# Performance work log

Hardware: AMD Instinct MI355X
Metric: run time of the kernel (lower is better)

Reference implementation:

```python
import jax, jax.numpy as jnp
import numpy as np

TEMP = 0.07
BASE_TEMP = 0.07
LOSS_WEIGHT = 0.5
BN_EPS = 1e-5

N, C_IN, H, W = 8, 512, 128, 128
FEAT_DIM = 256
N_ANCHOR, N_VIEW = 152, 26  # total_classes, n_view from max_samples=4096


def _embed(x, W1, b1, gamma, beta, W2, b2):
    # x: [N, C, H, W]; 1x1 conv -> BatchNorm (batch stats, training mode) -> ReLU -> 1x1 conv -> L2 norm over channel
    h = jnp.einsum('nchw,dc->ndhw', x, W1) + b1[None, :, None, None]
    mu = h.mean(axis=(0, 2, 3), keepdims=True)
    var = h.var(axis=(0, 2, 3), keepdims=True)
    h = (h - mu) * jax.lax.rsqrt(var + BN_EPS)
    h = h * gamma[None, :, None, None] + beta[None, :, None, None]
    h = jax.nn.relu(h)
    z = jnp.einsum('nchw,dc->ndhw', h, W2) + b2[None, :, None, None]
    nrm = jnp.sqrt(jnp.sum(z * z, axis=1, keepdims=True))
    return z / jnp.maximum(nrm, 1e-12)


def _contrastive(fS, fT, labels):
    # fS, fT: [A, V, d]; labels: [A]
    A, V, d = fS.shape
    anchor = jnp.transpose(fS, (1, 0, 2)).reshape(V * A, d)  # cat(unbind(dim=1))
    contrast = jax.lax.stop_gradient(jnp.transpose(fT, (1, 0, 2)).reshape(V * A, d))
    logits = (anchor @ contrast.T) / TEMP  # [M, M]
    logits = logits - jax.lax.stop_gradient(logits.max(axis=1, keepdims=True))
    base = (labels[:, None] == labels[None, :]).astype(logits.dtype)  # [A, A]
    mask = jnp.tile(base, (V, V))  # repeat(anchor_count, contrast_count)
    neg_mask = 1.0 - mask
    M = V * A
    mask = mask * (1.0 - jnp.eye(M, dtype=logits.dtype))  # remove self-pairs
    exp_l = jnp.exp(logits)
    neg = (exp_l * neg_mask).sum(axis=1, keepdims=True)
    log_prob = logits - jnp.log(exp_l + neg)
    mean_log_prob_pos = (mask * log_prob).sum(axis=1) / (mask.sum(axis=1) + 1e-6)
    return (-(TEMP / BASE_TEMP) * mean_log_prob_pos).mean()


def setup_inputs() -> dict:
    key = jax.random.key(0)
    ks = jax.random.split(key, 16)
    inp = {
        'preds_S': jax.random.normal(ks[0], (N, C_IN, H, W), jnp.float32),
        'preds_T': jax.random.normal(ks[1], (N, C_IN, H, W), jnp.float32),
        'sample_batch': jax.random.randint(ks[2], (N_ANCHOR,), 0, N, jnp.int32),
        'sample_idx': jax.random.randint(ks[3], (N_ANCHOR, N_VIEW), 0, H * W, jnp.int32),
        'labels_': jax.random.randint(ks[4], (N_ANCHOR,), 0, 19, jnp.int32),
    }
    def conv_params(k, cin, cout):
        k1, k2 = jax.random.split(k)
        return (jax.random.normal(k1, (cout, cin), jnp.float32) * 0.02,
                jnp.zeros((cout,), jnp.float32))
    for pfx, kw, kb in (('s', ks[5], ks[6]), ('t', ks[7], ks[8])):
        W1, b1 = conv_params(kw, C_IN, C_IN)
        W2, b2 = conv_params(kb, C_IN, FEAT_DIM)
        inp[f'{pfx}_W1'], inp[f'{pfx}_b1'] = W1, b1
        inp[f'{pfx}_gamma'] = jnp.ones((C_IN,), jnp.float32)
        inp[f'{pfx}_beta'] = jnp.zeros((C_IN,), jnp.float32)
        inp[f'{pfx}_W2'], inp[f'{pfx}_b2'] = W2, b2
    return inp


def reference(preds_S, preds_T, sample_batch, sample_idx, labels_,
              s_W1, s_b1, s_gamma, s_beta, s_W2, s_b2,
              t_W1, t_b1, t_gamma, t_beta, t_W2, t_b2):
    zS = _embed(preds_S, s_W1, s_b1, s_gamma, s_beta, s_W2, s_b2)
    zT = _embed(preds_T, t_W1, t_b1, t_gamma, t_beta, t_W2, t_b2)
    n, d, h, w = zS.shape
    fS = jnp.transpose(zS, (0, 2, 3, 1)).reshape(n, h * w, d)
    fT = jnp.transpose(zT, (0, 2, 3, 1)).reshape(n, h * w, d)
    # hard-anchor gather: [A, V, d]
    fS_ = fS[sample_batch[:, None], sample_idx]
    fT_ = fT[sample_batch[:, None], sample_idx]
    loss = _contrastive(fS_, fT_, labels_) + _contrastive(fT_, fS_, labels_)
    return LOSS_WEIGHT * loss
```

## Files before the change

### kernel.cpp

```cpp
#include <hip/hip_runtime.h>
#include <hip/hip_bf16.h>

#define A_N 152
#define V_N 26
#define M_N 3952
#define M_PAD 3968
#define CIN 512
#define FDIM 256
#define HW_SZ 16384
#define P_TOT 131072.0f
#define TEMP_INV 14.285714285714286f
#define NGRP 2048
#define LCAP 64
#define PCAP 768

typedef __attribute__((ext_vector_type(8))) short bf16x8;
typedef __attribute__((ext_vector_type(4))) float f32x4;

static __device__ __forceinline__ short f2bf(float x){
  union { float f; unsigned u; } v; v.f = x;
  unsigned r = (v.u + 0x7FFFu + ((v.u >> 16) & 1u)) >> 16;
  return (short)r;
}

static __device__ __forceinline__ bf16x8 ldfrag(const short* __restrict__ base, int ld,
                                                int row, int k, int lane){
  return *(const bf16x8*)(base + (size_t)(row + (lane & 15)) * ld + k + ((lane >> 4) << 3));
}

static __device__ __forceinline__ bf16x8 ldfragP(const short* __restrict__ base,
                                                 int dtile, int ktile, int lane){
  return *(const bf16x8*)(base + ((((size_t)dtile << 4) + ktile) << 9) + (lane << 3));
}

static __device__ __forceinline__ void cvt4(short* __restrict__ lds, float4 v,
                                            int px, int tid){
  lds[(px+0)*512 + (tid ^ (((px+0)&7)<<3))] = f2bf(v.x);
  lds[(px+1)*512 + (tid ^ (((px+1)&7)<<3))] = f2bf(v.y);
  lds[(px+2)*512 + (tid ^ (((px+2)&7)<<3))] = f2bf(v.z);
  lds[(px+3)*512 + (tid ^ (((px+3)&7)<<3))] = f2bf(v.w);
}

__global__ void castw_kernel(const float* __restrict__ a0, short* __restrict__ o0,
                             const float* __restrict__ a1, short* __restrict__ o1,
                             const float* __restrict__ a2, short* __restrict__ o2,
                             const float* __restrict__ a3, short* __restrict__ o3){
  const float* a; short* o; int n;
  switch (blockIdx.y){
    case 0: a = a0; o = o0; n = CIN*CIN; break;
    case 1: a = a1; o = o1; n = CIN*CIN; break;
    case 2: a = a2; o = o2; n = FDIM*CIN; break;
    default: a = a3; o = o3; n = FDIM*CIN; break;
  }
  int i = blockIdx.x * 256 + threadIdx.x;
  if (i >= n) return;
  if (blockIdx.y < 2){
    int j  = i & 7;
    int ln = (i >> 3) & 63;
    int kt = (i >> 9) & 15;
    int dt = i >> 13;
    int row = dt * 16 + (ln & 15);
    int col = kt * 32 + ((ln >> 4) << 3) + j;
    o[i] = f2bf(a[row * CIN + col]);
  } else {
    o[i] = f2bf(a[i]);
  }
}

__global__ __launch_bounds__(64) void build_lists_kernel(
    const int* __restrict__ sb, const int* __restrict__ si,
    int* __restrict__ counts, int* __restrict__ lists){
  int m = blockIdx.x * 64 + threadIdx.x;
  if (m >= M_N) return;
  int a = m % A_N, v = m / A_N;
  int pix = si[a * V_N + v];
  int g = sb[a] * 256 + (pix >> 6);
  int slot = atomicAdd(&counts[g], 1);
  if (slot < LCAP) lists[g * LCAP + slot] = m | ((pix & 63) << 16);
}

__global__ __launch_bounds__(512, 2) void stats_kernel(
    const float* __restrict__ xS, const float* __restrict__ xT,
    const short* __restrict__ w1S, const short* __restrict__ w1T,
    float* __restrict__ stats,
    const int* __restrict__ counts, const int* __restrict__ lists,
    short* __restrict__ xsS, short* __restrict__ xsT){
  __shared__ short lds[128 * 512];
  const int t = blockIdx.y;
  const float* __restrict__ x = t ? xT : xS;
  const short* __restrict__ w1 = t ? w1T : w1S;
  float* sums = stats + t * 1024;
  short* __restrict__ xs = t ? xsT : xsS;

  const int tid  = threadIdx.x;
  const int lane = tid & 63;
  const int wave = tid >> 6;

  float rs[4] = {0.f,0.f,0.f,0.f};
  float rq[4] = {0.f,0.f,0.f,0.f};

  for (int it = 0; it < 4; ++it){
    const int T   = blockIdx.x + it * 256;
    const int n   = T >> 7;
    const int hw0 = (T & 127) << 7;
    const float* src = x + ((size_t)(n * CIN + tid)) * HW_SZ + hw0;

    const int g0 = T * 2, g1 = g0 + 1;
    int cnt0 = counts[g0]; if (cnt0 > LCAP) cnt0 = LCAP;
    int cnt1 = counts[g1]; if (cnt1 > LCAP) cnt1 = LCAP;

    #pragma unroll
    for (int ch = 0; ch < 8; ++ch){
      float4 v0 = *(const float4*)(src + ch * 16 +  0);
      float4 v1 = *(const float4*)(src + ch * 16 +  4);
      float4 v2 = *(const float4*)(src + ch * 16 +  8);
      float4 v3 = *(const float4*)(src + ch * 16 + 12);
      cvt4(lds, v0, ch * 16 +  0, tid);
      cvt4(lds, v1, ch * 16 +  4, tid);
      cvt4(lds, v2, ch * 16 +  8, tid);
      cvt4(lds, v3, ch * 16 + 12, tid);
    }
    __syncthreads();

    f32x4 acc[8][4] = {};
    {
      bf16x8 c0 = ldfragP(w1, wave*4 + 0, 0, lane);
      bf16x8 c1 = ldfragP(w1, wave*4 + 1, 0, lane);
      bf16x8 c2 = ldfragP(w1, wave*4 + 2, 0, lane);
      bf16x8 c3 = ldfragP(w1, wave*4 + 3, 0, lane);
      for (int kt = 0; kt < 16; ++kt){
        const int kn = (kt + 1) & 15;
        bf16x8 n0 = ldfragP(w1, wave*4 + 0, kn, lane);
        bf16x8 n1 = ldfragP(w1, wave*4 + 1, kn, lane);
        bf16x8 n2 = ldfragP(w1, wave*4 + 2, kn, lane);
        bf16x8 n3 = ldfragP(w1, wave*4 + 3, kn, lane);
        const int kk = kt << 5;
        #pragma unroll
        for (int pi = 0; pi < 8; ++pi){
          int px = pi*16 + (lane & 15);
          int c  = (kk + ((lane >> 4) << 3)) ^ ((px & 7) << 3);
          bf16x8 af = *(const bf16x8*)(lds + px*512 + c);
          acc[pi][0] = __builtin_amdgcn_mfma_f32_16x16x32_bf16(af, c0, acc[pi][0], 0, 0, 0);
          acc[pi][1] = __builtin_amdgcn_mfma_f32_16x16x32_bf16(af, c1, acc[pi][1], 0, 0, 0);
          acc[pi][2] = __builtin_amdgcn_mfma_f32_16x16x32_bf16(af, c2, acc[pi][2], 0, 0, 0);
          acc[pi][3] = __builtin_amdgcn_mfma_f32_16x16x32_bf16(af, c3, acc[pi][3], 0, 0, 0);
        }
        c0 = n0; c1 = n1; c2 = n2; c3 = n3;
      }
    }
    #pragma unroll
    for (int di = 0; di < 4; ++di){
      float s = 0.f, q2 = 0.f;
      #pragma unroll
      for (int pi = 0; pi < 8; ++pi)
        #pragma unroll
        for (int r = 0; r < 4; ++r){ float vv = acc[pi][di][r]; s += vv; q2 += vv*vv; }
      rs[di] += s; rq[di] += q2;
    }

    for (int s = 0; s < cnt0; ++s){
      int e = lists[g0 * LCAP + s];
      int m = e & 0xFFFF, px = e >> 16;
      xs[(size_t)m * CIN + tid] = lds[px * 512 + (tid ^ ((px & 7) << 3))];
    }
    for (int s = 0; s < cnt1; ++s){
      int e = lists[g1 * LCAP + s];
      int m = e & 0xFFFF, px = (e >> 16) + 64;
      xs[(size_t)m * CIN + tid] = lds[px * 512 + (tid ^ ((px & 7) << 3))];
    }
    __syncthreads();
  }
  #pragma unroll
  for (int di = 0; di < 4; ++di){
    float s = rs[di], q2 = rq[di];
    s  += __shfl_xor(s, 16, 64);  s  += __shfl_xor(s, 32, 64);
    q2 += __shfl_xor(q2, 16, 64); q2 += __shfl_xor(q2, 32, 64);
    if ((lane & 48) == 0){
      int d = wave * 64 + di*16 + lane;
      atomicAdd(&sums[d], s);
      atomicAdd(&sums[512 + d], q2);
    }
  }
}

__global__ __launch_bounds__(256) void conv1_kernel(
    const short* __restrict__ xsS, const short* __restrict__ xsT,
    const short* __restrict__ w1S, const short* __restrict__ w1T,
    const float* __restrict__ stats,
    const float* __restrict__ gS, const float* __restrict__ bS,
    const float* __restrict__ gT, const float* __restrict__ bT,
    short* __restrict__ hrS, short* __restrict__ hrT){
  const int t = blockIdx.z;
  const short* xs = t ? xsT : xsS;
  const short* w1 = t ? w1T : w1S;
  const float* sums  = stats + t * 1024;
  const float* gamma = t ? gT : gS;
  const float* beta  = t ? bT : bS;
  short* hr = t ? hrT : hrS;

  const int lane = threadIdx.x & 63;
  const int wave = threadIdx.x >> 6;
  const int m0 = blockIdx.x * 16;
  const int dt0 = (blockIdx.y * 4 + wave) * 4;
  const int d0  = dt0 * 16;

  f32x4 acc[4] = {};
  for (int kk = 0; kk < CIN; kk += 32){
    bf16x8 a = ldfrag(xs, CIN, m0, kk, lane);
    #pragma unroll
    for (int di = 0; di < 4; ++di){
      bf16x8 b = ldfragP(w1, dt0 + di, kk >> 5, lane);
      acc[di] = __builtin_amdgcn_mfma_f32_16x16x32_bf16(a, b, acc[di], 0, 0, 0);
    }
  }
  const float invP = 1.f / P_TOT;
  #pragma unroll
  for (int di = 0; di < 4; ++di){
    int d = d0 + di*16 + (lane & 15);
    float mu  = sums[d] * invP;
    float var = sums[512 + d] * invP - mu * mu;
    float sc  = gamma[d] * rsqrtf(var + 1e-5f);
    float sh  = beta[d] - mu * sc;
    #pragma unroll
    for (int r = 0; r < 4; ++r){
      int m = m0 + ((lane >> 4) << 2) + r;
      float v = fmaxf(acc[di][r] * sc + sh, 0.f);
      hr[(size_t)m * CIN + d] = f2bf(v);
    }
  }
}

__global__ __launch_bounds__(256) void conv2_kernel(
    const short* __restrict__ hrS, const short* __restrict__ hrT,
    const short* __restrict__ w2S, const short* __restrict__ w2T,
    const float* __restrict__ b2S, const float* __restrict__ b2T,
    short* __restrict__ fS, short* __restrict__ fT){
  __shared__ float ssum[4][16];
  const int t = blockIdx.y;
  const short* hr = t ? hrT : hrS;
  const short* w2 = t ? w2T : w2S;
  const float* b2 = t ? b2T : b2S;
  short* f = t ? fT : fS;

  const int lane = threadIdx.x & 63;
  const int wave = threadIdx.x >> 6;
  const int m0 = blockIdx.x * 16;
  const int e0 = wave * 64;

  f32x4 acc[4] = {};
  for (int kk = 0; kk < CIN; kk += 32){
    bf16x8 a = ldfrag(hr, CIN, m0, kk, lane);
    #pragma unroll
    for (int ei = 0; ei < 4; ++ei){
      bf16x8 b = ldfrag(w2, CIN, e0 + ei*16, kk, lane);
      acc[ei] = __builtin_amdgcn_mfma_f32_16x16x32_bf16(a, b, acc[ei], 0, 0, 0);
    }
  }
  float z[4][4];
  float part[4] = {0.f,0.f,0.f,0.f};
  #pragma unroll
  for (int ei = 0; ei < 4; ++ei){
    int e = e0 + ei*16 + (lane & 15);
    float bb = b2[e];
    #pragma unroll
    for (int r = 0; r < 4; ++r){
      float v = acc[ei][r] + bb;
      z[ei][r] = v;
      part[r] += v * v;
    }
  }
  #pragma unroll
  for (int r = 0; r < 4; ++r){
    float p = part[r];
    p += __shfl_xor(p, 1, 64); p += __shfl_xor(p, 2, 64);
    p += __shfl_xor(p, 4, 64); p += __shfl_xor(p, 8, 64);
    part[r] = p;
  }
  if ((lane & 15) == 0){
    #pragma unroll
    for (int r = 0; r < 4; ++r) ssum[wave][((lane >> 4) << 2) + r] = part[r];
  }
  __syncthreads();
  #pragma unroll
  for (int r = 0; r < 4; ++r){
    int mrow = ((lane >> 4) << 2) + r;
    float tot = ssum[0][mrow] + ssum[1][mrow] + ssum[2][mrow] + ssum[3][mrow];
    float sc = 1.f / fmaxf(sqrtf(tot), 1e-12f);
    #pragma unroll
    for (int ei = 0; ei < 4; ++ei){
      int e = e0 + ei*16 + (lane & 15);
      f[(size_t)(m0 + mrow) * FDIM + e] = f2bf(z[ei][r] * sc);
    }
  }
}

__global__ __launch_bounds__(256) void fused_kernel(
    const short* __restrict__ fS, const short* __restrict__ fT,
    const int* __restrict__ labels, float* __restrict__ out){
  __shared__ unsigned char lab[M_N];
  __shared__ float stash[16][PCAP];
  __shared__ int   scnt[16];
  __shared__ float redm[4][16], reds[4][16];
  __shared__ float fmx[16], fng[16];

  const short* fa = blockIdx.y ? fT : fS;
  const short* fb = blockIdx.y ? fS : fT;
  const int tid  = threadIdx.x;
  const int lane = tid & 63;
  const int wave = tid >> 6;
  const int m0 = blockIdx.x * 16;

  for (int j = tid; j < M_N; j += 256) lab[j] = (unsigned char)labels[j % A_N];
  if (tid < 16) scnt[tid] = 0;
  __syncthreads();

  const int rbase = (lane >> 4) << 2;
  int labrow[4];
  #pragma unroll
  for (int r = 0; r < 4; ++r) labrow[r] = lab[m0 + rbase + r];

  float pm[4]   = {-3.4e38f,-3.4e38f,-3.4e38f,-3.4e38f};
  float psum[4] = {0.f,0.f,0.f,0.f};

  for (int nt = wave; nt < 62; nt += 4){
    const int n0 = nt * 64;
    f32x4 acc[4] = {};
    for (int kk = 0; kk < FDIM; kk += 32){
      bf16x8 a = ldfrag(fa, FDIM, m0, kk, lane);
      #pragma unroll
      for (int ni = 0; ni < 4; ++ni){
        bf16x8 b = ldfrag(fb, FDIM, n0 + ni*16, kk, lane);
        acc[ni] = __builtin_amdgcn_mfma_f32_16x16x32_bf16(a, b, acc[ni], 0, 0, 0);
      }
    }
    #pragma unroll
    for (int ni = 0; ni < 4; ++ni){
      int col = n0 + ni*16 + (lane & 15);
      if (col < M_N){
        int labc = lab[col];
        #pragma unroll
        for (int r = 0; r < 4; ++r){
          int rowg = m0 + rbase + r;
          if (col == rowg) continue;
          float l = acc[ni][r] * TEMP_INV;
          if (labc == labrow[r]){
            int slot = atomicAdd(&scnt[rbase + r], 1);
            if (slot < PCAP) stash[rbase + r][slot] = l;
          } else if (l > pm[r]){
            psum[r] = psum[r] * __expf(pm[r] - l) + 1.f;
            pm[r] = l;
          } else {
            psum[r] += __expf(l - pm[r]);
          }
        }
      }
    }
  }

  #pragma unroll
  for (int r = 0; r < 4; ++r){
    #pragma unroll
    for (int s = 1; s < 16; s <<= 1){
      float om = __shfl_xor(pm[r], s, 64);
      float os = __shfl_xor(psum[r], s, 64);
      float nm = fmaxf(pm[r], om);
      psum[r] = psum[r] * __expf(pm[r] - nm) + os * __expf(om - nm);
      pm[r] = nm;
    }
    if ((lane & 15) == 0){ redm[wave][rbase + r] = pm[r]; reds[wave][rbase + r] = psum[r]; }
  }
  __syncthreads();
  if (tid < 16){
    float m = redm[0][tid], s = reds[0][tid];
    #pragma unroll
    for (int w = 1; w < 4; ++w){
      float om = redm[w][tid], os = reds[w][tid];
      float nm = fmaxf(m, om);
      s = s * __expf(m - nm) + os * __expf(om - nm);
      m = nm;
    }
    fmx[tid] = m; fng[tid] = s;
  }
  __syncthreads();

  {
    const int rowl = tid >> 4;
    const int t16  = tid & 15;
    int cnt = scnt[rowl]; if (cnt > PCAP) cnt = PCAP;
    const float mx = fmx[rowl], neg = fng[rowl];
    float ps = 0.f;
    for (int s = t16; s < cnt; s += 16){
      float l = stash[rowl][s] - mx;
      ps += l - __logf(__expf(l) + neg);
    }
    #pragma unroll
    for (int s = 1; s < 16; s <<= 1) ps += __shfl_xor(ps, s, 64);
    if (t16 == 0){
      float mlpp = ps / ((float)cnt + 1e-6f);
      atomicAdd(out, -0.5f / (float)M_N * mlpp);
    }
  }
}

extern "C" void kernel_launch(void* const* d_in, const int* in_sizes, int n_in,
                              void* d_out, int out_size, void* d_ws, size_t ws_size,
                              hipStream_t stream){
  const float* xS     = (const float*)d_in[0];
  const float* xT     = (const float*)d_in[1];
  const int*   sb     = (const int*)d_in[2];
  const int*   si     = (const int*)d_in[3];
  const int*   labels = (const int*)d_in[4];
  const float* sW1    = (const float*)d_in[5];
  const float* sGamma = (const float*)d_in[7];
  const float* sBeta  = (const float*)d_in[8];
  const float* sW2    = (const float*)d_in[9];
  const float* sB2    = (const float*)d_in[10];
  const float* tW1    = (const float*)d_in[11];
  const float* tGamma = (const float*)d_in[13];
  const float* tBeta  = (const float*)d_in[14];
  const float* tW2    = (const float*)d_in[15];
  const float* tB2    = (const float*)d_in[16];
  float* out = (float*)d_out;

  char* ws = (char*)d_ws;
  size_t off = 0;
  auto alloc = [&](size_t bytes) -> void* {
    void* p = ws + off;
    off = (off + bytes + 255) & ~(size_t)255;
    return p;
  };
  short* w1bS = (short*)alloc((size_t)CIN * CIN * 2);
  short* w1bT = (short*)alloc((size_t)CIN * CIN * 2);
  short* w2bS = (short*)alloc((size_t)FDIM * CIN * 2);
  short* w2bT = (short*)alloc((size_t)FDIM * CIN * 2);
  float* stats = (float*)alloc(2 * 1024 * 4);
  int* counts = (int*)alloc(NGRP * 4);
  int* lists  = (int*)alloc((size_t)NGRP * LCAP * 4);
  short* xsS = (short*)alloc((size_t)M_N * CIN * 2);
  short* xsT = (short*)alloc((size_t)M_N * CIN * 2);
  short* hrS = (short*)alloc((size_t)M_N * CIN * 2);
  short* hrT = (short*)alloc((size_t)M_N * CIN * 2);
  short* fS  = (short*)alloc((size_t)M_PAD * FDIM * 2);
  short* fT  = (short*)alloc((size_t)M_PAD * FDIM * 2);

  (void)hipMemsetAsync(d_out, 0, sizeof(float), stream);
  (void)hipMemsetAsync(stats, 0, 2 * 1024 * 4, stream);
  (void)hipMemsetAsync(counts, 0, NGRP * 4, stream);
  (void)hipMemsetAsync(fS + (size_t)M_N * FDIM, 0, (size_t)(M_PAD - M_N) * FDIM * 2, stream);
  (void)hipMemsetAsync(fT + (size_t)M_N * FDIM, 0, (size_t)(M_PAD - M_N) * FDIM * 2, stream);

  castw_kernel<<<dim3((CIN*CIN + 255) / 256, 4), 256, 0, stream>>>(
      sW1, w1bS, tW1, w1bT, sW2, w2bS, tW2, w2bT);
  build_lists_kernel<<<dim3((M_N + 63) / 64), 64, 0, stream>>>(sb, si, counts, lists);

  stats_kernel<<<dim3(256, 2), 512, 0, stream>>>(xS, xT, w1bS, w1bT, stats,
                                                 counts, lists, xsS, xsT);
  conv1_kernel<<<dim3(247, 2, 2), 256, 0, stream>>>(xsS, xsT, w1bS, w1bT, stats,
                                                    sGamma, sBeta, tGamma, tBeta, hrS, hrT);
  conv2_kernel<<<dim3(247, 2), 256, 0, stream>>>(hrS, hrT, w2bS, w2bT, sB2, tB2, fS, fT);

  fused_kernel<<<dim3(247, 2), 256, 0, stream>>>(fS, fT, labels, out);
}
```

Measured before the change: 537.6 us.

## Use fixed logit shift and subtract positives from total exp sum

Replaces the online running-max softmax accumulation with a constant shift of 1/T, which is the upper bound on logits for unit-norm features. Every column's exp is summed without branching, and the negative sum is recovered by subtracting the positive and self exps afterwards. The W2 fragment load also switches to a pre-permuted layout, with the cast kernel permuting all weights. The risk is precision loss from cancellation when subtracting positive exps from the total, and the bf16-rounded norm could slightly exceed one.

After: 528.6 us. About the same (-1.7%).

```diff
diff --git a/kernel.cpp b/kernel.cpp
--- a/kernel.cpp
+++ b/kernel.cpp
@@ -10,6 +10,7 @@
 #define HW_SZ 16384
 #define P_TOT 131072.0f
 #define TEMP_INV 14.285714285714286f
+#define MSHIFT  14.285714285714286f
 #define NGRP 2048
 #define LCAP 64
 #define PCAP 768
@@ -54,17 +55,13 @@
   }
   int i = blockIdx.x * 256 + threadIdx.x;
   if (i >= n) return;
-  if (blockIdx.y < 2){
-    int j  = i & 7;
-    int ln = (i >> 3) & 63;
-    int kt = (i >> 9) & 15;
-    int dt = i >> 13;
-    int row = dt * 16 + (ln & 15);
-    int col = kt * 32 + ((ln >> 4) << 3) + j;
-    o[i] = f2bf(a[row * CIN + col]);
-  } else {
-    o[i] = f2bf(a[i]);
-  }
+  int j  = i & 7;
+  int ln = (i >> 3) & 63;
+  int kt = (i >> 9) & 15;
+  int dt = i >> 13;
+  int row = dt * 16 + (ln & 15);
+  int col = kt * 32 + ((ln >> 4) << 3) + j;
+  o[i] = f2bf(a[row * CIN + col]);
 }
 
 __global__ __launch_bounds__(64) void build_lists_kernel(
@@ -252,7 +249,7 @@
     bf16x8 a = ldfrag(hr, CIN, m0, kk, lane);
     #pragma unroll
     for (int ei = 0; ei < 4; ++ei){
-      bf16x8 b = ldfrag(w2, CIN, e0 + ei*16, kk, lane);
+      bf16x8 b = ldfragP(w2, wave*4 + ei, kk >> 5, lane);
       acc[ei] = __builtin_amdgcn_mfma_f32_16x16x32_bf16(a, b, acc[ei], 0, 0, 0);
     }
   }
@@ -300,8 +297,9 @@
   __shared__ unsigned char lab[M_N];
   __shared__ float stash[16][PCAP];
   __shared__ int   scnt[16];
-  __shared__ float redm[4][16], reds[4][16];
-  __shared__ float fmx[16], fng[16];
+  __shared__ float reds[4][16];
+  __shared__ float fng[16];
+  __shared__ float selfl[16];
 
   const short* fa = blockIdx.y ? fT : fS;
   const short* fb = blockIdx.y ? fS : fT;
@@ -319,7 +317,6 @@
   #pragma unroll
   for (int r = 0; r < 4; ++r) labrow[r] = lab[m0 + rbase + r];
 
-  float pm[4]   = {-3.4e38f,-3.4e38f,-3.4e38f,-3.4e38f};
   float psum[4] = {0.f,0.f,0.f,0.f};
 
   for (int nt = wave; nt < 62; nt += 4){
@@ -340,17 +337,16 @@
         int labc = lab[col];
         #pragma unroll
         for (int r = 0; r < 4; ++r){
-          int rowg = m0 + rbase + r;
-          if (col == rowg) continue;
           float l = acc[ni][r] * TEMP_INV;
+          psum[r] += __expf(l - MSHIFT);
           if (labc == labrow[r]){
-            int slot = atomicAdd(&scnt[rbase + r], 1);
-            if (slot < PCAP) stash[rbase + r][slot] = l;
-          } else if (l > pm[r]){
-            psum[r] = psum[r] * __expf(pm[r] - l) + 1.f;
-            pm[r] = l;
-          } else {
-            psum[r] += __expf(l - pm[r]);
+            int rowg = m0 + rbase + r;
+            if (col != rowg){
+              int slot = atomicAdd(&scnt[rbase + r], 1);
+              if (slot < PCAP) stash[rbase + r][slot] = l;
+            } else {
+              selfl[rbase + r] = l;
+            }
           }
         }
       }
@@ -360,37 +356,25 @@
   #pragma unroll
   for (int r = 0; r < 4; ++r){
     #pragma unroll
-    for (int s = 1; s < 16; s <<= 1){
-      float om = __shfl_xor(pm[r], s, 64);
-      float os = __shfl_xor(psum[r], s, 64);
-      float nm = fmaxf(pm[r], om);
-      psum[r] = psum[r] * __expf(pm[r] - nm) + os * __expf(om - nm);
-      pm[r] = nm;
-    }
-    if ((lane & 15) == 0){ redm[wave][rbase + r] = pm[r]; reds[wave][rbase + r] = psum[r]; }
+    for (int s = 1; s < 16; s <<= 1) psum[r] += __shfl_xor(psum[r], s, 64);
+    if ((lane & 15) == 0) reds[wave][rbase + r] = psum[r];
   }
   __syncthreads();
-  if (tid < 16){
-    float m = redm[0][tid], s = reds[0][tid];
-    #pragma unroll
-    for (int w = 1; w < 4; ++w){
-      float om = redm[w][tid], os = reds[w][tid];
-      float nm = fmaxf(m, om);
-      s = s * __expf(m - nm) + os * __expf(om - nm);
-      m = nm;
-    }
-    fmx[tid] = m; fng[tid] = s;
-  }
+  if (tid < 16) fng[tid] = reds[0][tid] + reds[1][tid] + reds[2][tid] + reds[3][tid];
   __syncthreads();
 
   {
     const int rowl = tid >> 4;
     const int t16  = tid & 15;
     int cnt = scnt[rowl]; if (cnt > PCAP) cnt = PCAP;
-    const float mx = fmx[rowl], neg = fng[rowl];
+    float pexp = 0.f;
+    for (int s = t16; s < cnt; s += 16) pexp += __expf(stash[rowl][s] - MSHIFT);
+    #pragma unroll
+    for (int s = 1; s < 16; s <<= 1) pexp += __shfl_xor(pexp, s, 64);
+    const float neg = fng[rowl] - pexp - __expf(selfl[rowl] - MSHIFT);
     float ps = 0.f;
     for (int s = t16; s < cnt; s += 16){
-      float l = stash[rowl][s] - mx;
+      float l = stash[rowl][s] - MSHIFT;
       ps += l - __logf(__expf(l) + neg);
     }
     #pragma unroll
```
